# Optimization experiments

Measured on AMD Instinct MI355X. Metric: run time of the kernel, lower is better.

Reference implementation:

```python
import jax, jax.numpy as jnp
import numpy as np

DIM = 128
H = 8
EXP = 4
INNER = EXP * DIM          # 512
HD = INNER // H            # 64
B, N = 4, 1024
PE_C = 32


def setup_inputs() -> dict:
    key = jax.random.key(0)
    ks = jax.random.split(key, 9)
    s = 0.02
    return {
        "x": jax.random.normal(ks[0], (B, N, DIM), jnp.float32),
        "pe": jax.random.normal(ks[1], (N, N, PE_C), jnp.float32),
        "Wq": jax.random.normal(ks[2], (INNER, DIM), jnp.float32) * s,
        "Wk": jax.random.normal(ks[3], (INNER, DIM), jnp.float32) * s,
        "Wv": jax.random.normal(ks[4], (INNER, DIM), jnp.float32) * s,
        "bv": jax.random.normal(ks[5], (INNER,), jnp.float32) * s,
        "Wproj": jax.random.normal(ks[6], (DIM, INNER), jnp.float32) * s,
        "Wpe": jax.random.normal(ks[7], (HD, PE_C), jnp.float32) * s,
        "bpe": jax.random.normal(ks[8], (HD,), jnp.float32) * s,
    }


def reference(x, pe, Wq, Wk, Wv, bv, Wproj, Wpe, bpe):
    Bsz, Nn, C = x.shape
    scale = HD ** (-0.5)
    # [B, N, inner] -> [B, H, N, hd]
    def split_heads(t):
        return t.reshape(Bsz, Nn, H, HD).transpose(0, 2, 1, 3)
    q = split_heads(x @ Wq.T)
    k = split_heads(x @ Wk.T)
    v = split_heads(x @ Wv.T + bv)
    score = jnp.einsum('bhic,bhjc->bhij', q * scale, k)   # [B,H,N,N]
    attn = jax.nn.softmax(score, axis=-1)
    out = jnp.einsum('bhij,bhjc->bhic', attn, v)           # [B,H,N,hd]
    pe_sum = jnp.einsum('bhij,ijc->bhic', attn, pe)        # [B,H,N,32]
    out = out + pe_sum @ Wpe.T + bpe                       # pe_proj
    out = out.transpose(0, 2, 1, 3).reshape(Bsz, Nn, H * HD)
    return out @ Wproj.T                                   # [B,N,dim]
```

## Files before the change

kernel.cpp:

```cpp
#include <hip/hip_runtime.h>
#include <hip/hip_bf16.h>

#define DIM   128
#define NH    8
#define INNER 512
#define HD    64
#define BSZ   4
#define NSEQ  1024
#define PEC   32
#define BH    32

typedef __attribute__((ext_vector_type(4))) float f32x4;
typedef __attribute__((ext_vector_type(2))) float f32x2;
typedef __attribute__((ext_vector_type(8))) short s16x8;
typedef __attribute__((ext_vector_type(4))) unsigned short u16x4;
typedef __attribute__((ext_vector_type(2))) unsigned int u32x2;

__device__ __forceinline__ unsigned short f2bf(float f) {
    unsigned u = __float_as_uint(f);
    u += 0x7fffu + ((u >> 16) & 1u);
    return (unsigned short)(u >> 16);
}

__device__ __forceinline__ float bf2f(short s) {
    return __uint_as_float(((unsigned)(unsigned short)s) << 16);
}

__device__ __forceinline__ s16x8 load8bf(const float* p) {
    f32x4 a = *(const f32x4*)p;
    f32x4 b = *(const f32x4*)(p + 4);
    s16x8 r;
    r[0] = (short)f2bf(a[0]); r[1] = (short)f2bf(a[1]);
    r[2] = (short)f2bf(a[2]); r[3] = (short)f2bf(a[3]);
    r[4] = (short)f2bf(b[0]); r[5] = (short)f2bf(b[1]);
    r[6] = (short)f2bf(b[2]); r[7] = (short)f2bf(b[3]);
    return r;
}

__device__ __forceinline__ f32x4 mfma16(s16x8 a, s16x8 b, f32x4 c) {
    return __builtin_amdgcn_mfma_f32_16x16x32_bf16(a, b, c, 0, 0, 0);
}

__global__ __launch_bounds__(256) void k_qkv(
    const float* __restrict__ x,
    const float* __restrict__ Wq, const float* __restrict__ Wk,
    const float* __restrict__ Wv, const float* __restrict__ bv,
    unsigned short* __restrict__ qws, unsigned short* __restrict__ kws,
    unsigned short* __restrict__ vtws)
{
    __shared__ unsigned short xs[64][136];
    int lane = threadIdx.x & 63, wave = threadIdx.x >> 6;
    int lr = lane & 15, lg = lane >> 4;
    int ct   = blockIdx.x * 4 + wave;
    int col0 = ct * 16;
    int m0   = blockIdx.y * 64;

    int tid = threadIdx.x;
    #pragma unroll
    for (int it = 0; it < 4; ++it) {
        int flat = it * 256 + tid;
        int r = flat >> 4, c8 = (flat & 15) * 8;
        *(s16x8*)&xs[r][c8] = load8bf(x + (m0 + r) * DIM + c8);
    }
    __syncthreads();

    const float* W; int cbase; int which = col0 >> 9;
    if (which == 0)      { W = Wq; cbase = col0; }
    else if (which == 1) { W = Wk; cbase = col0 - 512; }
    else                 { W = Wv; cbase = col0 - 1024; }

    const float* wrow = W + (cbase + lr) * DIM;
    s16x8 bfr[4];
    #pragma unroll
    for (int kt = 0; kt < 4; ++kt) bfr[kt] = load8bf(wrow + kt * 32 + lg * 8);

    if (which == 2) {
        int colW = cbase + lr;
        int h = colW >> 6, d = colW & 63;
        float bias = bv[colW];
        #pragma unroll
        for (int ms = 0; ms < 4; ++ms) {
            f32x4 acc = {0.f, 0.f, 0.f, 0.f};
            #pragma unroll
            for (int kt = 0; kt < 4; ++kt) {
                s16x8 a = *(const s16x8*)&xs[ms * 16 + lr][kt * 32 + lg * 8];
                acc = mfma16(a, bfr[kt], acc);
            }
            int mB = m0 + ms * 16 + lg * 4;
            int b  = mB >> 10;
            int bh = b * NH + h;
            u16x4 pk;
            #pragma unroll
            for (int v = 0; v < 4; ++v) pk[v] = f2bf(acc[v] + bias);
            int n0 = mB & 1023;
            *(u16x4*)(vtws + (bh * HD + d) * NSEQ + n0) = pk;
        }
    } else {
        int h = cbase >> 6;
        int dbase = (cbase & 63) + lg * 4;
        unsigned short* dst = (which == 0) ? qws : kws;
        float scale = (which == 0) ? 0.125f : 1.0f;
        #pragma unroll
        for (int ms = 0; ms < 4; ++ms) {
            f32x4 acc = {0.f, 0.f, 0.f, 0.f};
            #pragma unroll
            for (int kt = 0; kt < 4; ++kt) {
                s16x8 a = *(const s16x8*)&xs[ms * 16 + lr][kt * 32 + lg * 8];
                acc = mfma16(bfr[kt], a, acc);
            }
            int m = m0 + ms * 16 + lr;
            int b = m >> 10, n = m & 1023;
            int bh = b * NH + h;
            u16x4 pk;
            #pragma unroll
            for (int v = 0; v < 4; ++v) pk[v] = f2bf(acc[v] * scale);
            *(u16x4*)(dst + ((size_t)bh * NSEQ + n) * HD + dbase) = pk;
        }
    }
}

__global__ __launch_bounds__(256, 2) void k_fattn(
    const unsigned short* __restrict__ qws, const unsigned short* __restrict__ kws,
    const unsigned short* __restrict__ vtws,
    unsigned short* __restrict__ attnw, float* __restrict__ outv)
{
    __shared__ unsigned short Pl[32 * 1024];
    __shared__ float mlb[4][2][16][2];
    int lane = threadIdx.x & 63, wave = threadIdx.x >> 6;
    int lr = lane & 15, lg = lane >> 4;
    int L = blockIdx.x;
    int bh = (L & 7) * 4 + ((L >> 3) & 3);
    int i0 = (L >> 5) * 32;

    auto paddr = [&](int r, int jb) -> char* {
        unsigned mask = (unsigned)(((r & 7) << 4) | ((r & 3) << 7));
        return (char*)Pl + (unsigned)(r * 2048) + ((unsigned)jb ^ mask);
    };

    s16x8 qf[2][2];
    #pragma unroll
    for (int m = 0; m < 2; ++m) {
        const unsigned short* qrow = qws + (bh * NSEQ + i0 + m * 16 + lr) * HD;
        qf[m][0] = *(const s16x8*)(qrow + lg * 8);
        qf[m][1] = *(const s16x8*)(qrow + 32 + lg * 8);
    }

    f32x4 s[16][2];
    #pragma unroll
    for (int jc = 0; jc < 16; ++jc) {
        const unsigned short* krow =
            kws + (bh * NSEQ + wave * 256 + jc * 16 + lr) * HD + lg * 8;
        s16x8 kf0 = *(const s16x8*)(krow);
        s16x8 kf1 = *(const s16x8*)(krow + 32);
        #pragma unroll
        for (int m = 0; m < 2; ++m) {
            f32x4 acc = {0.f, 0.f, 0.f, 0.f};
            acc = mfma16(kf0, qf[m][0], acc);
            s[jc][m] = mfma16(kf1, qf[m][1], acc);
        }
    }

    float mx[2], sm[2];
    #pragma unroll
    for (int m = 0; m < 2; ++m) {
        float v = -3.0e38f;
        #pragma unroll
        for (int jc = 0; jc < 16; ++jc) {
            f32x4 t = s[jc][m];
            v = fmaxf(v, fmaxf(fmaxf(t[0], t[1]), fmaxf(t[2], t[3])));
        }
        v = fmaxf(v, __shfl_xor(v, 16));
        v = fmaxf(v, __shfl_xor(v, 32));
        mx[m] = v;
    }
    #pragma unroll
    for (int m = 0; m < 2; ++m) {
        float sum = 0.f;
        #pragma unroll
        for (int jc = 0; jc < 16; ++jc) {
            f32x4 t = s[jc][m];
            #pragma unroll
            for (int u = 0; u < 4; ++u) { t[u] = __expf(t[u] - mx[m]); sum += t[u]; }
            s[jc][m] = t;
        }
        sum += __shfl_xor(sum, 16);
        sum += __shfl_xor(sum, 32);
        sm[m] = sum;
    }
    if (lg == 0) {
        #pragma unroll
        for (int m = 0; m < 2; ++m) {
            mlb[wave][m][lr][0] = mx[m];
            mlb[wave][m][lr][1] = sm[m];
        }
    }
    __syncthreads();

    float f[2];
    #pragma unroll
    for (int m = 0; m < 2; ++m) {
        float M = -3.0e38f;
        #pragma unroll
        for (int w = 0; w < 4; ++w) M = fmaxf(M, mlb[w][m][lr][0]);
        float Ls = 0.f;
        #pragma unroll
        for (int w = 0; w < 4; ++w)
            Ls += mlb[w][m][lr][1] * __expf(mlb[w][m][lr][0] - M);
        f[m] = __expf(mx[m] - M) / Ls;
    }

    #pragma unroll
    for (int jc = 0; jc < 16; ++jc) {
        #pragma unroll
        for (int m = 0; m < 2; ++m) {
            f32x4 t = s[jc][m];
            unsigned lo = (unsigned)f2bf(t[0] * f[m]) | ((unsigned)f2bf(t[1] * f[m]) << 16);
            unsigned hi = (unsigned)f2bf(t[2] * f[m]) | ((unsigned)f2bf(t[3] * f[m]) << 16);
            u32x2 pk = {lo, hi};
            int r  = m * 16 + lr;
            int jb = (wave * 512) + (jc * 32) + (lg * 8);
            *(u32x2*)paddr(r, jb) = pk;
        }
    }
    __syncthreads();

    #pragma unroll
    for (int r8 = 0; r8 < 8; ++r8) {
        int r = wave * 8 + r8;
        unsigned short* grow = attnw + ((size_t)(i0 + r) * BH + bh) * NSEQ;
        #pragma unroll
        for (int half = 0; half < 2; ++half) {
            int j = half * 512 + lane * 8;
            s16x8 val = *(s16x8*)paddr(r, j * 2);
            *(s16x8*)(grow + j) = val;
        }
    }

    int d0 = wave * 16;
    const unsigned short* vrow = vtws + (bh * HD + d0 + lr) * NSEQ + lg * 8;
    f32x4 o0 = {0.f, 0.f, 0.f, 0.f};
    f32x4 o1 = {0.f, 0.f, 0.f, 0.f};
    #pragma unroll
    for (int kt = 0; kt < 32; ++kt) {
        s16x8 bf = *(const s16x8*)(vrow + kt * 32);
        s16x8 a0 = *(s16x8*)paddr(lr,      kt * 64 + lg * 16);
        s16x8 a1 = *(s16x8*)paddr(16 + lr, kt * 64 + lg * 16);
        o0 = mfma16(a0, bf, o0);
        o1 = mfma16(a1, bf, o1);
    }
    float* orow = outv + (bh * NSEQ + i0) * HD;
    #pragma unroll
    for (int v = 0; v < 4; ++v) {
        orow[(lg * 4 + v) * HD + d0 + lr]      = o0[v];
        orow[(16 + lg * 4 + v) * HD + d0 + lr] = o1[v];
    }
}

__global__ __launch_bounds__(256) void k_pe(
    const unsigned short* __restrict__ attnw, const float* __restrict__ pe,
    float* __restrict__ pes)
{
    __shared__ unsigned short pt[4][2][PEC][40];
    __shared__ float part[4][BH][PEC];
    int i = blockIdx.x;
    int lane = threadIdx.x & 63, wave = threadIdx.x >> 6;
    int lr = lane & 15, lg = lane >> 4;
    int jp = lane & 15, cg = lane >> 4;
    const float* pei = pe + (size_t)i * NSEQ * PEC;
    int jbase = wave * 256;

    s16x8 af[8][2];
    #pragma unroll
    for (int t = 0; t < 8; ++t) {
        #pragma unroll
        for (int mh = 0; mh < 2; ++mh) {
            const unsigned short* ap =
                attnw + ((size_t)i * BH + mh * 16 + lr) * NSEQ + jbase + t * 32 + lg * 8;
            af[t][mh] = *(const s16x8*)ap;
        }
    }

    f32x4 r0, r1, r2, r3;
    auto issue = [&](int t) {
        const float* s0 = pei + (size_t)(jbase + t * 32 + jp * 2) * PEC + cg * 8;
        r0 = *(const f32x4*)(s0);
        r1 = *(const f32x4*)(s0 + 4);
        r2 = *(const f32x4*)(s0 + PEC);
        r3 = *(const f32x4*)(s0 + PEC + 4);
    };
    auto commit = [&](int buf) {
        #pragma unroll
        for (int cc = 0; cc < 4; ++cc) {
            unsigned lo = f2bf(r0[cc]), hi = f2bf(r2[cc]);
            *(unsigned*)&pt[wave][buf][cg * 8 + cc][jp * 2] = lo | (hi << 16);
        }
        #pragma unroll
        for (int cc = 0; cc < 4; ++cc) {
            unsigned lo = f2bf(r1[cc]), hi = f2bf(r3[cc]);
            *(unsigned*)&pt[wave][buf][cg * 8 + 4 + cc][jp * 2] = lo | (hi << 16);
        }
    };

    f32x4 acc00 = {0.f,0.f,0.f,0.f}, acc01 = {0.f,0.f,0.f,0.f};
    f32x4 acc10 = {0.f,0.f,0.f,0.f}, acc11 = {0.f,0.f,0.f,0.f};

    issue(0); commit(0);
    issue(1);
    #pragma unroll
    for (int t = 0; t < 8; ++t) {
        int cur = t & 1;
        s16x8 bf0 = *(const s16x8*)&pt[wave][cur][lr][lg * 8];
        s16x8 bf1 = *(const s16x8*)&pt[wave][cur][16 + lr][lg * 8];
        acc00 = mfma16(af[t][0], bf0, acc00);
        acc01 = mfma16(af[t][0], bf1, acc01);
        acc10 = mfma16(af[t][1], bf0, acc10);
        acc11 = mfma16(af[t][1], bf1, acc11);
        if (t < 7) {
            commit(cur ^ 1);
            if (t < 6) issue(t + 2);
        }
    }

    #pragma unroll
    for (int v = 0; v < 4; ++v) {
        part[wave][lg * 4 + v][lr]           = acc00[v];
        part[wave][lg * 4 + v][16 + lr]      = acc01[v];
        part[wave][16 + lg * 4 + v][lr]      = acc10[v];
        part[wave][16 + lg * 4 + v][16 + lr] = acc11[v];
    }
    __syncthreads();

    int tid = threadIdx.x;
    int bh = tid >> 3, c0 = (tid & 7) * 4;
    f32x4 s = *(f32x4*)&part[0][bh][c0];
    #pragma unroll
    for (int w = 1; w < 4; ++w) {
        f32x4 q = *(f32x4*)&part[w][bh][c0];
        s[0] += q[0]; s[1] += q[1]; s[2] += q[2]; s[3] += q[3];
    }
    *(f32x4*)(pes + ((size_t)bh * NSEQ + i) * PEC + c0) = s;
}

__global__ __launch_bounds__(512) void k_out(
    const float* __restrict__ outv, const float* __restrict__ pes,
    const float* __restrict__ Wpe, const float* __restrict__ bpe,
    const float* __restrict__ Wproj, float* __restrict__ out)
{
    __shared__ float wpe_s[HD * PEC];
    __shared__ float bpe_s[HD];
    __shared__ unsigned short tl[16][520];
    int tid = threadIdx.x;
    for (int idx = tid; idx < HD * PEC; idx += 512) wpe_s[idx] = Wpe[idx];
    if (tid < HD) bpe_s[tid] = bpe[tid];
    __syncthreads();

    int m0 = blockIdx.x * 16;

    {
        int r  = tid >> 5;
        int o  = tid & 31;
        int d0 = (o & 7) * 8;
        int hp = o >> 3;
        int m  = m0 + r;
        int b  = m >> 10, n = m & 1023;
        #pragma unroll
        for (int hh = 0; hh < 2; ++hh) {
            int h  = hh * 4 + hp;
            int bh = b * NH + h;
            const float* prow = pes + ((size_t)bh * NSEQ + n) * PEC;
            float pr[PEC];
            #pragma unroll
            for (int c = 0; c < PEC; c += 4) {
                f32x4 t = *(const f32x4*)(prow + c);
                pr[c] = t[0]; pr[c+1] = t[1]; pr[c+2] = t[2]; pr[c+3] = t[3];
            }
            const float* ovp = outv + ((size_t)bh * NSEQ + n) * HD + d0;
            s16x8 pk;
            #pragma unroll
            for (int dd = 0; dd < 8; ++dd) {
                float acc = bpe_s[d0 + dd] + ovp[dd];
                const float* wr = &wpe_s[(d0 + dd) * PEC];
                #pragma unroll
                for (int c = 0; c < PEC; ++c) acc += pr[c] * wr[c];
                pk[dd] = (short)f2bf(acc);
            }
            *(s16x8*)&tl[r][h * HD + d0] = pk;
        }
    }
    __syncthreads();

    int lane = tid & 63, wave = tid >> 6;
    int lr = lane & 15, lg = lane >> 4;
    int n0 = wave * 16;
    const float* brow = Wproj + (n0 + lr) * INNER;
    f32x4 acc = {0.f, 0.f, 0.f, 0.f};
    #pragma unroll
    for (int kt = 0; kt < 16; ++kt) {
        s16x8 afr = *(const s16x8*)&tl[lr][kt * 32 + lg * 8];
        s16x8 bfr = load8bf(brow + kt * 32 + lg * 8);
        acc = mfma16(afr, bfr, acc);
    }
    #pragma unroll
    for (int v = 0; v < 4; ++v)
        out[(m0 + lg * 4 + v) * DIM + n0 + lr] = acc[v];
}

extern "C" void kernel_launch(void* const* d_in, const int* in_sizes, int n_in,
                              void* d_out, int out_size, void* d_ws, size_t ws_size,
                              hipStream_t stream)
{
    const float* x     = (const float*)d_in[0];
    const float* pe    = (const float*)d_in[1];
    const float* Wq    = (const float*)d_in[2];
    const float* Wk    = (const float*)d_in[3];
    const float* Wv    = (const float*)d_in[4];
    const float* bv    = (const float*)d_in[5];
    const float* Wproj = (const float*)d_in[6];
    const float* Wpe   = (const float*)d_in[7];
    const float* bpe   = (const float*)d_in[8];
    float* out = (float*)d_out;

    char* ws = (char*)d_ws;
    unsigned short* qws  = (unsigned short*)(ws);
    unsigned short* kws  = (unsigned short*)(ws + ( 4u << 20));
    unsigned short* vtws = (unsigned short*)(ws + ( 8u << 20));
    unsigned short* attn = (unsigned short*)(ws + (12u << 20));
    float*          outv = (float*)         (ws + (76u << 20));
    float*          pes  = (float*)         (ws + (84u << 20));

    k_qkv  <<<dim3(24, 64), 256, 0, stream>>>(x, Wq, Wk, Wv, bv, qws, kws, vtws);
    k_fattn<<<dim3(1024),   256, 0, stream>>>(qws, kws, vtws, attn, outv);
    k_pe   <<<dim3(1024),   256, 0, stream>>>(attn, pe, pes);
    k_out  <<<dim3(256),    512, 0, stream>>>(outv, pes, Wpe, bpe, Wproj, out);
}
```

Baseline: 125.7 us.

## Fuse positional-encoding contraction into flash attention kernel, drop attention matrix writeback

Removes the separate k_pe kernel and the global bf16 attention-probability buffer. Each attention block now computes the pe-weighted sum for its 32 query rows directly from the shared-memory probabilities, using scalar fp32 FMAs against pe loaded from global memory. This avoids writing and re-reading the full attention matrix. In exchange, the pe tensor is no longer shared across the 32 batch-heads and is re-read by every (b,h) block, which multiplies pe traffic. The MFMA-based contraction is also replaced by plain vector ALU work.

```diff
diff --git a/kernel.cpp b/kernel.cpp
--- a/kernel.cpp
+++ b/kernel.cpp
@@ -119,10 +119,10 @@
     }
 }
 
-__global__ __launch_bounds__(256, 2) void k_fattn(
+__global__ __launch_bounds__(256, 2) void k_fattn_pe(
     const unsigned short* __restrict__ qws, const unsigned short* __restrict__ kws,
-    const unsigned short* __restrict__ vtws,
-    unsigned short* __restrict__ attnw, float* __restrict__ outv)
+    const unsigned short* __restrict__ vtws, const float* __restrict__ pe,
+    float* __restrict__ outv, float* __restrict__ pes)
 {
     __shared__ unsigned short Pl[32 * 1024];
     __shared__ float mlb[4][2][16][2];
@@ -224,18 +224,6 @@
     }
     __syncthreads();
 
-    #pragma unroll
-    for (int r8 = 0; r8 < 8; ++r8) {
-        int r = wave * 8 + r8;
-        unsigned short* grow = attnw + ((size_t)(i0 + r) * BH + bh) * NSEQ;
-        #pragma unroll
-        for (int half = 0; half < 2; ++half) {
-            int j = half * 512 + lane * 8;
-            s16x8 val = *(s16x8*)paddr(r, j * 2);
-            *(s16x8*)(grow + j) = val;
-        }
-    }
-
     int d0 = wave * 16;
     const unsigned short* vrow = vtws + (bh * HD + d0 + lr) * NSEQ + lg * 8;
     f32x4 o0 = {0.f, 0.f, 0.f, 0.f};
@@ -254,91 +242,35 @@
         orow[(lg * 4 + v) * HD + d0 + lr]      = o0[v];
         orow[(16 + lg * 4 + v) * HD + d0 + lr] = o1[v];
     }
-}
-
-__global__ __launch_bounds__(256) void k_pe(
-    const unsigned short* __restrict__ attnw, const float* __restrict__ pe,
-    float* __restrict__ pes)
-{
-    __shared__ unsigned short pt[4][2][PEC][40];
-    __shared__ float part[4][BH][PEC];
-    int i = blockIdx.x;
-    int lane = threadIdx.x & 63, wave = threadIdx.x >> 6;
-    int lr = lane & 15, lg = lane >> 4;
-    int jp = lane & 15, cg = lane >> 4;
-    const float* pei = pe + (size_t)i * NSEQ * PEC;
-    int jbase = wave * 256;
-
-    s16x8 af[8][2];
-    #pragma unroll
-    for (int t = 0; t < 8; ++t) {
-        #pragma unroll
-        for (int mh = 0; mh < 2; ++mh) {
-            const unsigned short* ap =
-                attnw + ((size_t)i * BH + mh * 16 + lr) * NSEQ + jbase + t * 32 + lg * 8;
-            af[t][mh] = *(const s16x8*)ap;
-        }
-    }
-
-    f32x4 r0, r1, r2, r3;
-    auto issue = [&](int t) {
-        const float* s0 = pei + (size_t)(jbase + t * 32 + jp * 2) * PEC + cg * 8;
-        r0 = *(const f32x4*)(s0);
-        r1 = *(const f32x4*)(s0 + 4);
-        r2 = *(const f32x4*)(s0 + PEC);
-        r3 = *(const f32x4*)(s0 + PEC + 4);
-    };
-    auto commit = [&](int buf) {
-        #pragma unroll
-        for (int cc = 0; cc < 4; ++cc) {
-            unsigned lo = f2bf(r0[cc]), hi = f2bf(r2[cc]);
-            *(unsigned*)&pt[wave][buf][cg * 8 + cc][jp * 2] = lo | (hi << 16);
-        }
-        #pragma unroll
-        for (int cc = 0; cc < 4; ++cc) {
-            unsigned lo = f2bf(r1[cc]), hi = f2bf(r3[cc]);
-            *(unsigned*)&pt[wave][buf][cg * 8 + 4 + cc][jp * 2] = lo | (hi << 16);
-        }
-    };
-
-    f32x4 acc00 = {0.f,0.f,0.f,0.f}, acc01 = {0.f,0.f,0.f,0.f};
-    f32x4 acc10 = {0.f,0.f,0.f,0.f}, acc11 = {0.f,0.f,0.f,0.f};
-
-    issue(0); commit(0);
-    issue(1);
-    #pragma unroll
-    for (int t = 0; t < 8; ++t) {
-        int cur = t & 1;
-        s16x8 bf0 = *(const s16x8*)&pt[wave][cur][lr][lg * 8];
-        s16x8 bf1 = *(const s16x8*)&pt[wave][cur][16 + lr][lg * 8];
-        acc00 = mfma16(af[t][0], bf0, acc00);
-        acc01 = mfma16(af[t][0], bf1, acc01);
-        acc10 = mfma16(af[t][1], bf0, acc10);
-        acc11 = mfma16(af[t][1], bf1, acc11);
-        if (t < 7) {
-            commit(cur ^ 1);
-            if (t < 6) issue(t + 2);
-        }
-    }
-
-    #pragma unroll
-    for (int v = 0; v < 4; ++v) {
-        part[wave][lg * 4 + v][lr]           = acc00[v];
-        part[wave][lg * 4 + v][16 + lr]      = acc01[v];
-        part[wave][16 + lg * 4 + v][lr]      = acc10[v];
-        part[wave][16 + lg * 4 + v][16 + lr] = acc11[v];
-    }
-    __syncthreads();
-
-    int tid = threadIdx.x;
-    int bh = tid >> 3, c0 = (tid & 7) * 4;
-    f32x4 s = *(f32x4*)&part[0][bh][c0];
-    #pragma unroll
-    for (int w = 1; w < 4; ++w) {
-        f32x4 q = *(f32x4*)&part[w][bh][c0];
-        s[0] += q[0]; s[1] += q[1]; s[2] += q[2]; s[3] += q[3];
-    }
-    *(f32x4*)(pes + ((size_t)bh * NSEQ + i) * PEC + c0) = s;
+
+    {
+        int tid = threadIdx.x;
+        int r  = tid >> 3;
+        int c0 = (tid & 7) * 4;
+        const float* per = pe + ((size_t)(i0 + r) * NSEQ) * PEC + c0;
+        f32x4 pa = {0.f, 0.f, 0.f, 0.f};
+        for (int jb8 = 0; jb8 < 128; ++jb8) {
+            s16x8 pv = *(s16x8*)paddr(r, jb8 * 16);
+            f32x4 w0 = *(const f32x4*)(per + (size_t)(jb8 * 8 + 0) * PEC);
+            f32x4 w1 = *(const f32x4*)(per + (size_t)(jb8 * 8 + 1) * PEC);
+            f32x4 w2 = *(const f32x4*)(per + (size_t)(jb8 * 8 + 2) * PEC);
+            f32x4 w3 = *(const f32x4*)(per + (size_t)(jb8 * 8 + 3) * PEC);
+            f32x4 w4 = *(const f32x4*)(per + (size_t)(jb8 * 8 + 4) * PEC);
+            f32x4 w5 = *(const f32x4*)(per + (size_t)(jb8 * 8 + 5) * PEC);
+            f32x4 w6 = *(const f32x4*)(per + (size_t)(jb8 * 8 + 6) * PEC);
+            f32x4 w7 = *(const f32x4*)(per + (size_t)(jb8 * 8 + 7) * PEC);
+            float p0 = bf2f(pv[0]), p1 = bf2f(pv[1]);
+            float p2 = bf2f(pv[2]), p3 = bf2f(pv[3]);
+            float p4 = bf2f(pv[4]), p5 = bf2f(pv[5]);
+            float p6 = bf2f(pv[6]), p7 = bf2f(pv[7]);
+            #pragma unroll
+            for (int v = 0; v < 4; ++v) {
+                pa[v] += p0 * w0[v] + p1 * w1[v] + p2 * w2[v] + p3 * w3[v]
+                       + p4 * w4[v] + p5 * w5[v] + p6 * w6[v] + p7 * w7[v];
+            }
+        }
+        *(f32x4*)(pes + ((size_t)bh * NSEQ + (i0 + r)) * PEC + c0) = pa;
+    }
 }
 
 __global__ __launch_bounds__(512) void k_out(
@@ -424,12 +356,10 @@
     unsigned short* qws  = (unsigned short*)(ws);
     unsigned short* kws  = (unsigned short*)(ws + ( 4u << 20));
     unsigned short* vtws = (unsigned short*)(ws + ( 8u << 20));
-    unsigned short* attn = (unsigned short*)(ws + (12u << 20));
-    float*          outv = (float*)         (ws + (76u << 20));
-    float*          pes  = (float*)         (ws + (84u << 20));
-
-    k_qkv  <<<dim3(24, 64), 256, 0, stream>>>(x, Wq, Wk, Wv, bv, qws, kws, vtws);
-    k_fattn<<<dim3(1024),   256, 0, stream>>>(qws, kws, vtws, attn, outv);
-    k_pe   <<<dim3(1024),   256, 0, stream>>>(attn, pe, pes);
-    k_out  <<<dim3(256),    512, 0, stream>>>(outv, pes, Wpe, bpe, Wproj, out);
-}
+    float*          outv = (float*)         (ws + (12u << 20));
+    float*          pes  = (float*)         (ws + (20u << 20));
+
+    k_qkv     <<<dim3(24, 64), 256, 0, stream>>>(x, Wq, Wk, Wv, bv, qws, kws, vtws);
+    k_fattn_pe<<<dim3(1024),   256, 0, stream>>>(qws, kws, vtws, pe, outv, pes);
+    k_out     <<<dim3(256),    512, 0, stream>>>(outv, pes, Wpe, bpe, Wproj, out);
+}
```

Measured after the change: 252.7 us. 101% more time.
